# Kernel optimization log

Measured on AMD Instinct MI355X. Metric: run time of the kernel, lower is better.

Reference implementation:

```python
import jax, jax.numpy as jnp
import numpy as np
import math

N_HEADS = 16
EMBED = 1024
D_HEAD = EMBED // N_HEADS
B, L = 2, 2048


def setup_inputs() -> dict:
    key = jax.random.key(0)
    k1, k2, k3, k4, k5 = jax.random.split(key, 5)
    s = 0.02
    return {
        "x": jax.random.normal(k1, (B, L, EMBED), dtype=jnp.float32),
        "w_qkv": jax.random.normal(k2, (3 * EMBED, EMBED), dtype=jnp.float32) * s,
        "b_qkv": jax.random.normal(k3, (3 * EMBED,), dtype=jnp.float32) * s,
        "w_out": jax.random.normal(k4, (EMBED, EMBED), dtype=jnp.float32) * s,
        "b_out": jax.random.normal(k5, (EMBED,), dtype=jnp.float32) * s,
        "mask": 1,
    }


def reference(x, w_qkv, b_qkv, w_out, b_out, mask):
    b, l, e = x.shape
    qkv = x @ w_qkv.T + b_qkv                      # (B, L, 3E)
    q, k, v = jnp.split(qkv, 3, axis=-1)
    # (B, L, H, d) -> (B, H, L, d)
    q = q.reshape(b, l, N_HEADS, D_HEAD).transpose(0, 2, 1, 3)
    k = k.reshape(b, l, N_HEADS, D_HEAD).transpose(0, 2, 1, 3)
    v = v.reshape(b, l, N_HEADS, D_HEAD).transpose(0, 2, 1, 3)
    # NOTE: faithful to source bug -- scores use V, not K
    scores = jnp.einsum("bhld,bhmd->bhlm", q, v) * (1.0 / math.sqrt(D_HEAD))
    if mask:
        causal = jnp.triu(jnp.ones((l, l), dtype=bool), k=1)  # (L, L)
        scores = jnp.where(causal, -jnp.inf, scores)
    attn = jax.nn.softmax(scores, axis=-1)          # (B, H, L, L)
    out = jnp.einsum("bhlm,bhmd->bhld", attn, v)    # (B, H, L, d)
    # NOTE: faithful to source bug -- transpose(1,2) result discarded,
    # so reshape straight from (B, H, L, d) to (B, L, E)
    out = out.reshape(b, l, e)
    return out @ w_out.T + b_out
```

## Files before the change

kernel.cpp:

```cpp
#include <hip/hip_runtime.h>
#include <math.h>

constexpr int Lc = 2048, Ec = 1024, Hc = 16, Dc = 64;

typedef __attribute__((ext_vector_type(8))) short bf16x8;
typedef __attribute__((ext_vector_type(4))) float f32x4;
typedef unsigned short u16;
typedef unsigned int u32;

#define MFMA16(a, b, c) __builtin_amdgcn_mfma_f32_16x16x32_bf16(a, b, c, 0, 0, 0)

__device__ inline u16 f2bf(float f) {
  u32 u = __builtin_bit_cast(u32, f);
  u32 r = u + 0x7fff + ((u >> 16) & 1);
  return (u16)(r >> 16);
}

__device__ inline void gld16(const void* g, void* l) {
  __builtin_amdgcn_global_load_lds(
      (const __attribute__((address_space(1))) u32*)g,
      (__attribute__((address_space(3))) u32*)l, 16, 0, 0);
}

constexpr size_t XN = (size_t)4096 * 1024;
constexpr size_t WQN = (size_t)2048 * 1024;
constexpr size_t WON = (size_t)1024 * 1024;

__global__ __launch_bounds__(256) void convert_all(
    const float* __restrict__ x, const float* __restrict__ wqkv,
    const float* __restrict__ wout, u16* __restrict__ xb,
    u16* __restrict__ wqb, u16* __restrict__ wob)
{
  const size_t i = ((size_t)blockIdx.x * 256 + threadIdx.x) * 4;
  float4 v;
  u16* dst;
  if (i < XN) {
    v = *(const float4*)(x + i);
    dst = xb + i;
  } else if (i < XN + WQN) {
    const size_t off = i - XN;
    const size_t row = off >> 10, col = off & 1023;
    const size_t srow = row + ((row >> 10) << 10);
    v = *(const float4*)(wqkv + srow * 1024 + col);
    dst = wqb + off;
  } else {
    const size_t off = i - XN - WQN;
    v = *(const float4*)(wout + off);
    dst = wob + off;
  }
  u16 o0 = f2bf(v.x), o1 = f2bf(v.y), o2 = f2bf(v.z), o3 = f2bf(v.w);
  dst[0] = o0; dst[1] = o1; dst[2] = o2; dst[3] = o3;
}

__global__ __launch_bounds__(256) void transpose_v(
    const u16* __restrict__ V, u16* __restrict__ Vt)
{
  __shared__ __align__(16) u16 T[64][72];
  const int bh = blockIdx.y, lt = blockIdx.x * 64;
  const int r = threadIdx.x >> 2;
  const int c = (threadIdx.x & 3) * 16;
  const u16* src = V + ((size_t)bh * Lc + lt) * Dc;
  *(bf16x8*)&T[r][c]     = *(const bf16x8*)(src + (size_t)r * 64 + c);
  *(bf16x8*)&T[r][c + 8] = *(const bf16x8*)(src + (size_t)r * 64 + c + 8);
  __syncthreads();
  bf16x8 o0, o1;
#pragma unroll
  for (int j = 0; j < 8; ++j) o0[j] = (short)T[c + j][r];
#pragma unroll
  for (int j = 0; j < 8; ++j) o1[j] = (short)T[c + 8 + j][r];
  u16* dst = Vt + ((size_t)bh * Dc + r) * Lc + lt + c;
  *(bf16x8*)dst = o0;
  *(bf16x8*)(dst + 8) = o1;
}

__global__ __launch_bounds__(256) void gemm_qv(
    const u16* __restrict__ A, const u16* __restrict__ W,
    const float* __restrict__ bqkv, u16* __restrict__ Q, u16* __restrict__ V)
{
  __shared__ __align__(16) u16 As[2][4096];
  __shared__ __align__(16) u16 Bs[2][4096];
  const int tid = threadIdx.x;
  const int w = tid >> 6, lane = tid & 63;
  const int quad = lane >> 4, l16 = lane & 15;
  const int wm = w >> 1, wn = w & 1;
  const int rowTile = blockIdx.y * 128;
  const int colTile = blockIdx.x * 128;

  const int r0 = tid >> 2, o0 = (tid & 3) * 8;
  const u16* Ab0 = A + (size_t)(rowTile + r0) * 1024 + o0;
  const u16* Ab1 = Ab0 + (size_t)64 * 1024;
  const u16* Bb0 = W + (size_t)(colTile + r0) * 1024 + o0;
  const u16* Bb1 = Bb0 + (size_t)64 * 1024;

  f32x4 acc[4][4] = {};

  gld16(Ab0, &As[0][tid * 8]);
  gld16(Ab1, &As[0][2048 + tid * 8]);
  gld16(Bb0, &Bs[0][tid * 8]);
  gld16(Bb1, &Bs[0][2048 + tid * 8]);

  int cur = 0;
  for (int k0 = 0; k0 < 1024; k0 += 32) {
    __syncthreads();
    if (k0 + 32 < 1024) {
      const int sb = cur ^ 1, kn = k0 + 32;
      gld16(Ab0 + kn, &As[sb][tid * 8]);
      gld16(Ab1 + kn, &As[sb][2048 + tid * 8]);
      gld16(Bb0 + kn, &Bs[sb][tid * 8]);
      gld16(Bb1 + kn, &Bs[sb][2048 + tid * 8]);
    }
    bf16x8 af[4], bf[4];
#pragma unroll
    for (int s = 0; s < 4; ++s)
      af[s] = *(const bf16x8*)&As[cur][(wm * 64 + s * 16 + l16) * 32 + quad * 8];
#pragma unroll
    for (int n = 0; n < 4; ++n)
      bf[n] = *(const bf16x8*)&Bs[cur][(wn * 64 + n * 16 + l16) * 32 + quad * 8];
#pragma unroll
    for (int s = 0; s < 4; ++s)
#pragma unroll
      for (int n = 0; n < 4; ++n)
        acc[s][n] = MFMA16(af[s], bf[n], acc[s][n]);
    cur ^= 1;
  }

#pragma unroll
  for (int n = 0; n < 4; ++n) {
    const int gn = colTile + wn * 64 + n * 16 + l16;
    const bool isV = gn >= 1024;
    const float bias = bqkv[gn + (isV ? 1024 : 0)];
    const float scl = isV ? 1.0f : 0.125f;
    const int h = (gn & 1023) >> 6, d = gn & 63;
    u16* dst = isV ? V : Q;
#pragma unroll
    for (int s = 0; s < 4; ++s) {
#pragma unroll
      for (int r = 0; r < 4; ++r) {
        const int gm = rowTile + wm * 64 + s * 16 + quad * 4 + r;
        const int b = gm >> 11, l = gm & 2047;
        dst[(((size_t)(b * Hc + h)) * Lc + l) * Dc + d] = f2bf((acc[s][n][r] + bias) * scl);
      }
    }
  }
}

constexpr int PSTR = 72;

__device__ inline void attn_half(
    const bf16x8 qf[2], const bf16x8 bv[4][2], const bf16x8 bvt[4][2],
    u16* __restrict__ Ps, f32x4 O[4], float lsum[4],
    int kt, int wq, bool needmask, int quad, int l16)
{
  f32x4 sf[4] = {};
#pragma unroll
  for (int nb = 0; nb < 4; ++nb) {
    sf[nb] = MFMA16(qf[0], bv[nb][0], sf[nb]);
    sf[nb] = MFMA16(qf[1], bv[nb][1], sf[nb]);
  }
#pragma unroll
  for (int nb = 0; nb < 4; ++nb)
#pragma unroll
    for (int r = 0; r < 4; ++r) {
      float p = __expf(sf[nb][r]);
      if (needmask) {
        const int key = kt + nb * 16 + l16;
        const int qr = wq + quad * 4 + r;
        if (key > qr) p = 0.f;
      }
      lsum[r] += p;
      Ps[(quad * 4 + r) * PSTR + nb * 16 + l16] = f2bf(p);
    }
  bf16x8 pf[2];
#pragma unroll
  for (int kk = 0; kk < 2; ++kk)
    pf[kk] = *(const bf16x8*)&Ps[l16 * PSTR + kk * 32 + quad * 8];
#pragma unroll
  for (int db = 0; db < 4; ++db) {
    O[db] = MFMA16(pf[0], bvt[db][0], O[db]);
    O[db] = MFMA16(pf[1], bvt[db][1], O[db]);
  }
}

__global__ __launch_bounds__(256) void attn_mfma(
    const u16* __restrict__ Q, const u16* __restrict__ V,
    const u16* __restrict__ Vt, u16* __restrict__ outA)
{
  __shared__ __align__(16) u16 lds[2 * 4096 + 2 * 4096 + 2 * 4 * 16 * PSTR];
  const int tid = threadIdx.x;
  const int w = tid >> 6, lane = tid & 63;
  const int quad = lane >> 4, l16 = lane & 15;

  const int flat = blockIdx.x;
  const int xcd = flat & 7, slot = flat >> 3;
  const int bh = xcd * 4 + (slot >> 4);
  const int xblk = slot & 15;
  const int b = bh >> 4, h = bh & 15;

  const u16* Qb = Q + (size_t)bh * Lc * Dc;
  const u16* Vb = V + (size_t)bh * Lc * Dc;
  const u16* Vtb = Vt + (size_t)bh * Dc * Lc;
  u16* Psl = &lds[16384 + w * 16 * PSTR];
  u16* Psh = &lds[16384 + (4 + w) * 16 * PSTR];

  const int b1 = tid * 16, b2 = b1 + 4096;
  const int e1 = (b1 ^ (((b1 >> 7) & 7) << 4)) >> 1;
  const int e2 = (b2 ^ (((b2 >> 7) & 7) << 4)) >> 1;
  const u16* vs1 = Vb + e1;
  const u16* vs2 = Vb + e2;
  const u16* ts1 = Vtb + (size_t)(e1 >> 6) * Lc + (e1 & 63);
  const u16* ts2 = Vtb + (size_t)(e2 >> 6) * Lc + (e2 & 63);

  int roff[4][2];
#pragma unroll
  for (int i = 0; i < 4; ++i)
#pragma unroll
    for (int kk = 0; kk < 2; ++kk) {
      const int byte = ((i * 16 + l16) << 7) + kk * 64 + quad * 16;
      roff[i][kk] = (byte ^ ((l16 & 7) << 4)) >> 1;
    }

  const int qlo = xblk, qhi = 31 - xblk;
  const int nt = qhi + 1;
  const int wqlo = qlo * 64 + w * 16;
  const int wqhi = qhi * 64 + w * 16;

  bf16x8 qfl[2], qfh[2];
#pragma unroll
  for (int kk = 0; kk < 2; ++kk) {
    qfl[kk] = *(const bf16x8*)(Qb + (size_t)(qlo * 64 + w * 16 + l16) * 64 + kk * 32 + quad * 8);
    qfh[kk] = *(const bf16x8*)(Qb + (size_t)(qhi * 64 + w * 16 + l16) * 64 + kk * 32 + quad * 8);
  }

  f32x4 Ol[4] = {}, Oh[4] = {};
  float lsl[4] = {0.f, 0.f, 0.f, 0.f}, lsh[4] = {0.f, 0.f, 0.f, 0.f};

  gld16(vs1, &lds[tid * 8]);
  gld16(vs2, &lds[2048 + tid * 8]);
  gld16(ts1, &lds[8192 + tid * 8]);
  gld16(ts2, &lds[8192 + 2048 + tid * 8]);

  int cur = 0;
  for (int t = 0; t < nt; ++t) {
    const int kt = t * 64;
    __syncthreads();
    if (t + 1 < nt) {
      const int sb = cur ^ 1, nk = kt + 64;
      gld16(vs1 + (size_t)nk * 64, &lds[sb * 4096 + tid * 8]);
      gld16(vs2 + (size_t)nk * 64, &lds[sb * 4096 + 2048 + tid * 8]);
      gld16(ts1 + nk, &lds[8192 + sb * 4096 + tid * 8]);
      gld16(ts2 + nk, &lds[8192 + sb * 4096 + 2048 + tid * 8]);
    }
    const u16* VsB = &lds[cur * 4096];
    const u16* VtB = &lds[8192 + cur * 4096];

    bf16x8 bv[4][2], bvt[4][2];
#pragma unroll
    for (int nb = 0; nb < 4; ++nb)
#pragma unroll
      for (int kk = 0; kk < 2; ++kk) {
        bv[nb][kk] = *(const bf16x8*)(VsB + roff[nb][kk]);
        bvt[nb][kk] = *(const bf16x8*)(VtB + roff[nb][kk]);
      }

    attn_half(qfh, bv, bvt, Psh, Oh, lsh, kt, wqhi, t == qhi, quad, l16);
    if (t <= qlo)
      attn_half(qfl, bv, bvt, Psl, Ol, lsl, kt, wqlo, t == qlo, quad, l16);
    cur ^= 1;
  }

#pragma unroll
  for (int half = 0; half < 2; ++half) {
    const int q0 = half ? qhi * 64 : qlo * 64;
    const f32x4* O = half ? Oh : Ol;
    const float* ls = half ? lsh : lsl;
#pragma unroll
    for (int r = 0; r < 4; ++r) {
      float l = ls[r];
      l += __shfl_xor(l, 1);
      l += __shfl_xor(l, 2);
      l += __shfl_xor(l, 4);
      l += __shfl_xor(l, 8);
      const float inv = 1.f / l;
      const int q = q0 + w * 16 + quad * 4 + r;
      const int orow = h * 128 + (q >> 4);
      const int cbase = (q & 15) << 6;
#pragma unroll
      for (int db = 0; db < 4; ++db)
        outA[((size_t)b * Lc + orow) * Ec + cbase + db * 16 + l16] =
            f2bf(O[db][r] * inv);
    }
  }
}

__global__ __launch_bounds__(256) void gemm_out(
    const u16* __restrict__ A, const u16* __restrict__ W,
    const float* __restrict__ bias, float* __restrict__ out)
{
  __shared__ __align__(16) u16 As[2][4096];
  __shared__ __align__(16) u16 Bs[2][4096];
  const int tid = threadIdx.x;
  const int w = tid >> 6, lane = tid & 63;
  const int quad = lane >> 4, l16 = lane & 15;
  const int wm = w >> 1, wn = w & 1;
  const int rowTile = blockIdx.y * 128;
  const int colTile = blockIdx.x * 128;

  const int r0 = tid >> 2, o0 = (tid & 3) * 8;
  const u16* Ab0 = A + (size_t)(rowTile + r0) * 1024 + o0;
  const u16* Ab1 = Ab0 + (size_t)64 * 1024;
  const u16* Bb0 = W + (size_t)(colTile + r0) * 1024 + o0;
  const u16* Bb1 = Bb0 + (size_t)64 * 1024;

  f32x4 acc[4][4] = {};

  gld16(Ab0, &As[0][tid * 8]);
  gld16(Ab1, &As[0][2048 + tid * 8]);
  gld16(Bb0, &Bs[0][tid * 8]);
  gld16(Bb1, &Bs[0][2048 + tid * 8]);

  int cur = 0;
  for (int k0 = 0; k0 < 1024; k0 += 32) {
    __syncthreads();
    if (k0 + 32 < 1024) {
      const int sb = cur ^ 1, kn = k0 + 32;
      gld16(Ab0 + kn, &As[sb][tid * 8]);
      gld16(Ab1 + kn, &As[sb][2048 + tid * 8]);
      gld16(Bb0 + kn, &Bs[sb][tid * 8]);
      gld16(Bb1 + kn, &Bs[sb][2048 + tid * 8]);
    }
    bf16x8 af[4], bf[4];
#pragma unroll
    for (int s = 0; s < 4; ++s)
      af[s] = *(const bf16x8*)&As[cur][(wm * 64 + s * 16 + l16) * 32 + quad * 8];
#pragma unroll
    for (int n = 0; n < 4; ++n)
      bf[n] = *(const bf16x8*)&Bs[cur][(wn * 64 + n * 16 + l16) * 32 + quad * 8];
#pragma unroll
    for (int s = 0; s < 4; ++s)
#pragma unroll
      for (int n = 0; n < 4; ++n)
        acc[s][n] = MFMA16(af[s], bf[n], acc[s][n]);
    cur ^= 1;
  }

#pragma unroll
  for (int n = 0; n < 4; ++n) {
    const int gn = colTile + wn * 64 + n * 16 + l16;
    const float bn = bias[gn];
#pragma unroll
    for (int s = 0; s < 4; ++s)
#pragma unroll
      for (int r = 0; r < 4; ++r) {
        const int gm = rowTile + wm * 64 + s * 16 + quad * 4 + r;
        out[(size_t)gm * 1024 + gn] = acc[s][n][r] + bn;
      }
  }
}

extern "C" void kernel_launch(void* const* d_in, const int* in_sizes, int n_in,
                              void* d_out, int out_size, void* d_ws, size_t ws_size,
                              hipStream_t stream) {
  (void)in_sizes; (void)n_in; (void)out_size; (void)ws_size;
  const float* x     = (const float*)d_in[0];
  const float* w_qkv = (const float*)d_in[1];
  const float* b_qkv = (const float*)d_in[2];
  const float* w_out = (const float*)d_in[3];
  const float* b_out = (const float*)d_in[4];
  float* out = (float*)d_out;

  u16* xb  = (u16*)d_ws;
  u16* wqb = xb + XN;
  u16* wob = wqb + WQN;
  u16* Qw  = wob + WON;
  u16* Vw  = Qw + (size_t)2 * Hc * Lc * Dc;
  u16* Vtw = Vw + (size_t)2 * Hc * Lc * Dc;
  u16* Aw  = Vtw + (size_t)2 * Hc * Lc * Dc;

  convert_all<<<7168, 256, 0, stream>>>(x, w_qkv, w_out, xb, wqb, wob);
  gemm_qv<<<dim3(16, 32), 256, 0, stream>>>(xb, wqb, b_qkv, Qw, Vw);
  transpose_v<<<dim3(32, 32), 256, 0, stream>>>(Vw, Vtw);
  attn_mfma<<<512, 256, 0, stream>>>(Qw, Vw, Vtw, Aw);
  gemm_out<<<dim3(8, 32), 256, 0, stream>>>(Aw, wob, b_out, out);
}
```

Baseline: 176.1 us.

## Widen GEMM K-step to 64 with XOR-swizzled LDS and smaller out-proj tiles

Both projection GEMMs now stage 64-wide K slices instead of 32, which halves the number of barrier-synchronized loop iterations. The LDS layout is XOR-swizzled on 16-byte chunks so that the MFMA fragment reads avoid bank conflicts. The output GEMM switches to 64-row tiles, doubling its grid to 512 blocks so the CUs are better filled. In exchange, LDS use per block doubles, which may reduce occupancy.

New measurement: 176.2 us. No clear change (+0.1%).

```diff
diff --git a/kernel.cpp b/kernel.cpp
--- a/kernel.cpp
+++ b/kernel.cpp
@@ -77,8 +77,8 @@
     const u16* __restrict__ A, const u16* __restrict__ W,
     const float* __restrict__ bqkv, u16* __restrict__ Q, u16* __restrict__ V)
 {
-  __shared__ __align__(16) u16 As[2][4096];
-  __shared__ __align__(16) u16 Bs[2][4096];
+  __shared__ __align__(16) u16 As[2][8192];
+  __shared__ __align__(16) u16 Bs[2][8192];
   const int tid = threadIdx.x;
   const int w = tid >> 6, lane = tid & 63;
   const int quad = lane >> 4, l16 = lane & 15;
@@ -86,43 +86,53 @@
   const int rowTile = blockIdx.y * 128;
   const int colTile = blockIdx.x * 128;
 
-  const int r0 = tid >> 2, o0 = (tid & 3) * 8;
-  const u16* Ab0 = A + (size_t)(rowTile + r0) * 1024 + o0;
-  const u16* Ab1 = Ab0 + (size_t)64 * 1024;
-  const u16* Bb0 = W + (size_t)(colTile + r0) * 1024 + o0;
-  const u16* Bb1 = Bb0 + (size_t)64 * 1024;
+  const int srow = tid >> 3;
+  const int e = (((tid & 7) * 16) ^ ((srow & 7) << 4)) >> 1;
+  const u16* Asrc = A + (size_t)(rowTile + srow) * 1024 + e;
+  const u16* Bsrc = W + (size_t)(colTile + srow) * 1024 + e;
 
   f32x4 acc[4][4] = {};
 
-  gld16(Ab0, &As[0][tid * 8]);
-  gld16(Ab1, &As[0][2048 + tid * 8]);
-  gld16(Bb0, &Bs[0][tid * 8]);
-  gld16(Bb1, &Bs[0][2048 + tid * 8]);
-
+#define STAGE_QV(sb, k0)                                              \
+  {                                                                   \
+    gld16(Asrc + (k0),             &As[sb][tid * 8]);                 \
+    gld16(Asrc + (k0) + 32 * 1024, &As[sb][tid * 8 + 2048]);          \
+    gld16(Asrc + (k0) + 64 * 1024, &As[sb][tid * 8 + 4096]);          \
+    gld16(Asrc + (k0) + 96 * 1024, &As[sb][tid * 8 + 6144]);          \
+    gld16(Bsrc + (k0),             &Bs[sb][tid * 8]);                 \
+    gld16(Bsrc + (k0) + 32 * 1024, &Bs[sb][tid * 8 + 2048]);          \
+    gld16(Bsrc + (k0) + 64 * 1024, &Bs[sb][tid * 8 + 4096]);          \
+    gld16(Bsrc + (k0) + 96 * 1024, &Bs[sb][tid * 8 + 6144]);          \
+  }
+
+  STAGE_QV(0, 0);
   int cur = 0;
-  for (int k0 = 0; k0 < 1024; k0 += 32) {
+  for (int k0 = 0; k0 < 1024; k0 += 64) {
     __syncthreads();
-    if (k0 + 32 < 1024) {
-      const int sb = cur ^ 1, kn = k0 + 32;
-      gld16(Ab0 + kn, &As[sb][tid * 8]);
-      gld16(Ab1 + kn, &As[sb][2048 + tid * 8]);
-      gld16(Bb0 + kn, &Bs[sb][tid * 8]);
-      gld16(Bb1 + kn, &Bs[sb][2048 + tid * 8]);
-    }
-    bf16x8 af[4], bf[4];
+    if (k0 + 64 < 1024) STAGE_QV(cur ^ 1, k0 + 64);
+    bf16x8 af[4][2], bf[4][2];
 #pragma unroll
     for (int s = 0; s < 4; ++s)
-      af[s] = *(const bf16x8*)&As[cur][(wm * 64 + s * 16 + l16) * 32 + quad * 8];
+#pragma unroll
+      for (int kk = 0; kk < 2; ++kk)
+        af[s][kk] = *(const bf16x8*)&As[cur][(wm * 64 + s * 16 + l16) * 64 +
+                     ((kk * 32 + quad * 8) ^ ((l16 & 7) << 3))];
 #pragma unroll
     for (int n = 0; n < 4; ++n)
-      bf[n] = *(const bf16x8*)&Bs[cur][(wn * 64 + n * 16 + l16) * 32 + quad * 8];
-#pragma unroll
-    for (int s = 0; s < 4; ++s)
-#pragma unroll
-      for (int n = 0; n < 4; ++n)
-        acc[s][n] = MFMA16(af[s], bf[n], acc[s][n]);
+#pragma unroll
+      for (int kk = 0; kk < 2; ++kk)
+        bf[n][kk] = *(const bf16x8*)&Bs[cur][(wn * 64 + n * 16 + l16) * 64 +
+                     ((kk * 32 + quad * 8) ^ ((l16 & 7) << 3))];
+#pragma unroll
+    for (int kk = 0; kk < 2; ++kk)
+#pragma unroll
+      for (int s = 0; s < 4; ++s)
+#pragma unroll
+        for (int n = 0; n < 4; ++n)
+          acc[s][n] = MFMA16(af[s][kk], bf[n][kk], acc[s][n]);
     cur ^= 1;
   }
+#undef STAGE_QV
 
 #pragma unroll
   for (int n = 0; n < 4; ++n) {
@@ -297,61 +307,69 @@
     const float* __restrict__ bias, float* __restrict__ out)
 {
   __shared__ __align__(16) u16 As[2][4096];
-  __shared__ __align__(16) u16 Bs[2][4096];
+  __shared__ __align__(16) u16 Bs[2][8192];
   const int tid = threadIdx.x;
   const int w = tid >> 6, lane = tid & 63;
   const int quad = lane >> 4, l16 = lane & 15;
   const int wm = w >> 1, wn = w & 1;
-  const int rowTile = blockIdx.y * 128;
+  const int rowTile = blockIdx.y * 64;
   const int colTile = blockIdx.x * 128;
 
-  const int r0 = tid >> 2, o0 = (tid & 3) * 8;
-  const u16* Ab0 = A + (size_t)(rowTile + r0) * 1024 + o0;
-  const u16* Ab1 = Ab0 + (size_t)64 * 1024;
-  const u16* Bb0 = W + (size_t)(colTile + r0) * 1024 + o0;
-  const u16* Bb1 = Bb0 + (size_t)64 * 1024;
-
-  f32x4 acc[4][4] = {};
-
-  gld16(Ab0, &As[0][tid * 8]);
-  gld16(Ab1, &As[0][2048 + tid * 8]);
-  gld16(Bb0, &Bs[0][tid * 8]);
-  gld16(Bb1, &Bs[0][2048 + tid * 8]);
-
+  const int srow = tid >> 3;
+  const int e = (((tid & 7) * 16) ^ ((srow & 7) << 4)) >> 1;
+  const u16* Asrc = A + (size_t)(rowTile + srow) * 1024 + e;
+  const u16* Bsrc = W + (size_t)(colTile + srow) * 1024 + e;
+
+  f32x4 acc[2][4] = {};
+
+#define STAGE_OUT(sb, k0)                                             \
+  {                                                                   \
+    gld16(Asrc + (k0),             &As[sb][tid * 8]);                 \
+    gld16(Asrc + (k0) + 32 * 1024, &As[sb][tid * 8 + 2048]);          \
+    gld16(Bsrc + (k0),             &Bs[sb][tid * 8]);                 \
+    gld16(Bsrc + (k0) + 32 * 1024, &Bs[sb][tid * 8 + 2048]);          \
+    gld16(Bsrc + (k0) + 64 * 1024, &Bs[sb][tid * 8 + 4096]);          \
+    gld16(Bsrc + (k0) + 96 * 1024, &Bs[sb][tid * 8 + 6144]);          \
+  }
+
+  STAGE_OUT(0, 0);
   int cur = 0;
-  for (int k0 = 0; k0 < 1024; k0 += 32) {
+  for (int k0 = 0; k0 < 1024; k0 += 64) {
     __syncthreads();
-    if (k0 + 32 < 1024) {
-      const int sb = cur ^ 1, kn = k0 + 32;
-      gld16(Ab0 + kn, &As[sb][tid * 8]);
-      gld16(Ab1 + kn, &As[sb][2048 + tid * 8]);
-      gld16(Bb0 + kn, &Bs[sb][tid * 8]);
-      gld16(Bb1 + kn, &Bs[sb][2048 + tid * 8]);
-    }
-    bf16x8 af[4], bf[4];
-#pragma unroll
-    for (int s = 0; s < 4; ++s)
-      af[s] = *(const bf16x8*)&As[cur][(wm * 64 + s * 16 + l16) * 32 + quad * 8];
+    if (k0 + 64 < 1024) STAGE_OUT(cur ^ 1, k0 + 64);
+    bf16x8 af[2][2], bf[4][2];
+#pragma unroll
+    for (int s = 0; s < 2; ++s)
+#pragma unroll
+      for (int kk = 0; kk < 2; ++kk)
+        af[s][kk] = *(const bf16x8*)&As[cur][(wm * 32 + s * 16 + l16) * 64 +
+                     ((kk * 32 + quad * 8) ^ ((l16 & 7) << 3))];
 #pragma unroll
     for (int n = 0; n < 4; ++n)
-      bf[n] = *(const bf16x8*)&Bs[cur][(wn * 64 + n * 16 + l16) * 32 + quad * 8];
-#pragma unroll
-    for (int s = 0; s < 4; ++s)
-#pragma unroll
-      for (int n = 0; n < 4; ++n)
-        acc[s][n] = MFMA16(af[s], bf[n], acc[s][n]);
+#pragma unroll
+      for (int kk = 0; kk < 2; ++kk)
+        bf[n][kk] = *(const bf16x8*)&Bs[cur][(wn * 64 + n * 16 + l16) * 64 +
+                     ((kk * 32 + quad * 8) ^ ((l16 & 7) << 3))];
+#pragma unroll
+    for (int kk = 0; kk < 2; ++kk)
+#pragma unroll
+      for (int s = 0; s < 2; ++s)
+#pragma unroll
+        for (int n = 0; n < 4; ++n)
+          acc[s][n] = MFMA16(af[s][kk], bf[n][kk], acc[s][n]);
     cur ^= 1;
   }
+#undef STAGE_OUT
 
 #pragma unroll
   for (int n = 0; n < 4; ++n) {
     const int gn = colTile + wn * 64 + n * 16 + l16;
     const float bn = bias[gn];
 #pragma unroll
-    for (int s = 0; s < 4; ++s)
+    for (int s = 0; s < 2; ++s)
 #pragma unroll
       for (int r = 0; r < 4; ++r) {
-        const int gm = rowTile + wm * 64 + s * 16 + quad * 4 + r;
+        const int gm = rowTile + wm * 32 + s * 16 + quad * 4 + r;
         out[(size_t)gm * 1024 + gn] = acc[s][n][r] + bn;
       }
   }
@@ -380,5 +398,5 @@
   gemm_qv<<<dim3(16, 32), 256, 0, stream>>>(xb, wqb, b_qkv, Qw, Vw);
   transpose_v<<<dim3(32, 32), 256, 0, stream>>>(Vw, Vtw);
   attn_mfma<<<512, 256, 0, stream>>>(Qw, Vw, Vtw, Aw);
-  gemm_out<<<dim3(8, 32), 256, 0, stream>>>(Aw, wob, b_out, out);
-}
+  gemm_out<<<dim3(8, 64), 256, 0, stream>>>(Aw, wob, b_out, out);
+}
```
